# Performance work log

Hardware: AMD Instinct MI355X
Metric: run time of the kernel (lower is better)

Reference implementation:

```python
import jax, jax.numpy as jnp
import numpy as np

B, S, D, O, H, E, K = 4, 1024, 1024, 1024, 2048, 8, 2
EPS = 1e-5

def _layernorm(x, g, b):
    m = jnp.mean(x, axis=-1, keepdims=True)
    v = jnp.mean(jnp.square(x - m), axis=-1, keepdims=True)
    return (x - m) * jax.lax.rsqrt(v + EPS) * g + b

def setup_inputs() -> dict:
    key = jax.random.key(0)
    ks = jax.random.split(key, 8)
    def xavier(k, shape):
        fan_out, fan_in = shape[-2], shape[-1]
        bound = float(np.sqrt(6.0 / (fan_in + fan_out)))
        return jax.random.uniform(k, shape, jnp.float32, -bound, bound)
    return {
        "x": jax.random.normal(ks[0], (B, S, D), jnp.float32),
        "ln1_g": jnp.ones((D,), jnp.float32), "ln1_b": jnp.zeros((D,), jnp.float32),
        "router_w": xavier(ks[1], (E, D)), "router_b": jnp.zeros((E,), jnp.float32),
        "sh_w1": xavier(ks[2], (H, D)), "sh_b1": jnp.zeros((H,), jnp.float32),
        "sh_w2": xavier(ks[3], (O, H)), "sh_b2": jnp.zeros((O,), jnp.float32),
        "e_w1": xavier(ks[4], (E, H, D)), "e_b1": jnp.zeros((E, H), jnp.float32),
        "e_w2": xavier(ks[5], (E, O, H)), "e_b2": jnp.zeros((E, O), jnp.float32),
        "ln2_g": jnp.ones((O,), jnp.float32), "ln2_b": jnp.zeros((O,), jnp.float32),
    }

def reference(x, ln1_g, ln1_b, router_w, router_b, sh_w1, sh_b1, sh_w2, sh_b2,
              e_w1, e_b1, e_w2, e_b2, ln2_g, ln2_b):
    # eval mode: no router noise, no aux loss
    x_norm = _layernorm(x, ln1_g, ln1_b)               # [B,S,D]
    xf = x_norm.reshape(-1, D)                          # [T,D]
    logits = xf @ router_w.T + router_b                 # [T,E]
    probs = jax.nn.softmax(logits, axis=-1)
    tk_w, tk_i = jax.lax.top_k(probs, K)                # [T,K]
    tk_w = tk_w / jnp.sum(tk_w, axis=-1, keepdims=True)
    # shared expert (exact GELU, as torch nn.GELU default)
    shared = jax.nn.gelu(xf @ sh_w1.T + sh_b1, approximate=False) @ sh_w2.T + sh_b2  # [T,O]
    # all experts densely, combined sparsely by top-k weights
    hid = jax.nn.gelu(jnp.einsum('td,ehd->teh', xf, e_w1) + e_b1, approximate=False)  # [T,E,H]
    eout = jnp.einsum('teh,eoh->teo', hid, e_w2) + e_b2                                # [T,E,O]
    comb_w = jnp.sum(jax.nn.one_hot(tk_i, E, dtype=xf.dtype) * tk_w[..., None], axis=1)  # [T,E]
    out = shared * (1.0 / (E + 1)) + jnp.einsum('te,teo->to', comb_w, eout)           # [T,O]
    out = _layernorm(out.reshape(B, S, O), ln2_g, ln2_b)
    return out
```

## Files before the change

### kernel.cpp

```cpp
#include <hip/hip_runtime.h>
#include <math.h>
#include <stdint.h>

typedef unsigned short u16;
typedef unsigned int u32;

typedef __attribute__((ext_vector_type(8))) short bf16x8;
typedef __attribute__((ext_vector_type(4))) float f32x4;

#define ASYNC_COPY16(g, l)                                                         \
  __builtin_amdgcn_global_load_lds((__attribute__((address_space(1))) const void*)(g), \
                                   (__attribute__((address_space(3))) void*)(l), 16, 0, 0)

__device__ __forceinline__ float bf2f(u16 u) {
  union { u32 i; float f; } v; v.i = ((u32)u) << 16; return v.f;
}
__device__ __forceinline__ u16 f2bf(float f) {
  union { float f; u32 i; } v; v.f = f;
  u32 r = v.i + 0x7fffu + ((v.i >> 16) & 1u);
  return (u16)(r >> 16);
}

__global__ __launch_bounds__(256) void cvt_all_k(
    const float* __restrict__ s0, const float* __restrict__ s1,
    const float* __restrict__ s2, const float* __restrict__ s3,
    u16* __restrict__ dst)
{
  const int64_t i0 = (int64_t)blockIdx.x * 2048 + (int64_t)threadIdx.x * 8;
  const float* src; int64_t rel;
  if (i0 < 2097152)       { src = s0; rel = i0; }
  else if (i0 < 4194304)  { src = s1; rel = i0 - 2097152; }
  else if (i0 < 20971520) { src = s2; rel = i0 - 4194304; }
  else                    { src = s3; rel = i0 - 20971520; }
  const float4 a = *(const float4*)(src + rel);
  const float4 b = *(const float4*)(src + rel + 4);
  union { u16 h[8]; uint4 v; } o;
  o.h[0] = f2bf(a.x); o.h[1] = f2bf(a.y); o.h[2] = f2bf(a.z); o.h[3] = f2bf(a.w);
  o.h[4] = f2bf(b.x); o.h[5] = f2bf(b.y); o.h[6] = f2bf(b.z); o.h[7] = f2bf(b.w);
  *(uint4*)(dst + i0) = o.v;
}

__global__ __launch_bounds__(256) void ln_router_k(
    const float* __restrict__ x, const float* __restrict__ g, const float* __restrict__ b,
    const float* __restrict__ rw, const float* __restrict__ rb,
    u16* __restrict__ xn, int* __restrict__ tk_idx, float* __restrict__ tk_w)
{
  const int t = blockIdx.x, tid = threadIdx.x;
  __shared__ float xs[1024];
  __shared__ float red[8];
  __shared__ float logits[8];
  const int wave = tid >> 6, lane = tid & 63;

  const float4 xv = *(const float4*)(x + (size_t)t * 1024 + 4 * tid);
  float v0 = xv.x, v1 = xv.y, v2 = xv.z, v3 = xv.w;
  float s = v0 + v1 + v2 + v3;
  float q = v0 * v0 + v1 * v1 + v2 * v2 + v3 * v3;
#pragma unroll
  for (int o = 32; o > 0; o >>= 1) { s += __shfl_down(s, o, 64); q += __shfl_down(q, o, 64); }
  if (lane == 0) { red[wave] = s; red[4 + wave] = q; }
  __syncthreads();
  if (tid == 0) {
    float S = red[0] + red[1] + red[2] + red[3];
    float Q = red[4] + red[5] + red[6] + red[7];
    float mean = S * (1.0f / 1024.0f);
    float var = Q * (1.0f / 1024.0f) - mean * mean;
    red[0] = mean; red[1] = rsqrtf(var + 1e-5f);
  }
  __syncthreads();
  const float mean = red[0], rstd = red[1];
  float vv[4] = {v0, v1, v2, v3};
  union { u16 h[4]; uint2 v; } pk;
#pragma unroll
  for (int j = 0; j < 4; ++j) {
    int d = 4 * tid + j;
    float y = (vv[j] - mean) * rstd * g[d] + b[d];
    xs[d] = y;
    pk.h[j] = f2bf(y);
  }
  *(uint2*)(xn + (size_t)t * 1024 + 4 * tid) = pk.v;
  __syncthreads();
#pragma unroll
  for (int pe = 0; pe < 2; ++pe) {
    int e = wave + 4 * pe;
    const float* wrow = rw + (size_t)e * 1024;
    float acc = 0.f;
#pragma unroll
    for (int j = 0; j < 16; ++j) {
      int d = lane + 64 * j;
      acc += xs[d] * wrow[d];
    }
#pragma unroll
    for (int o = 32; o > 0; o >>= 1) acc += __shfl_down(acc, o, 64);
    if (lane == 0) logits[e] = acc + rb[e];
  }
  __syncthreads();
  if (tid == 0) {
    int i0 = 0; float l0 = logits[0];
#pragma unroll
    for (int e = 1; e < 8; ++e) if (logits[e] > l0) { l0 = logits[e]; i0 = e; }
    int i1 = -1; float l1 = -3.4e38f;
#pragma unroll
    for (int e = 0; e < 8; ++e) { if (e == i0) continue; if (logits[e] > l1) { l1 = logits[e]; i1 = e; } }
    float w0 = 1.0f / (1.0f + expf(l1 - l0));
    float w1 = 1.0f - w0;
    tk_idx[2 * t] = i0; tk_idx[2 * t + 1] = i1;
    tk_w[2 * t] = w0; tk_w[2 * t + 1] = w1;
  }
}

__device__ __forceinline__ uint4 u4_add(uint4 a, uint4 b) {
  uint4 r; r.x = a.x + b.x; r.y = a.y + b.y; r.z = a.z + b.z; r.w = a.w + b.w; return r;
}
__device__ __forceinline__ uint4 u4_sub(uint4 a, uint4 b) {
  uint4 r; r.x = a.x - b.x; r.y = a.y - b.y; r.z = a.z - b.z; r.w = a.w - b.w; return r;
}

__global__ __launch_bounds__(256) void assign_k(
    const int* __restrict__ tk_idx, const float* __restrict__ tk_w,
    int* __restrict__ offs, int* __restrict__ slot_token,
    float* __restrict__ slot_w, int* __restrict__ slot_of)
{
  const int tid = threadIdx.x, lane = tid & 63, wave = tid >> 6;
  int eidx[32];
#pragma unroll
  for (int j = 0; j < 32; ++j) eidx[j] = tk_idx[tid * 32 + j];

  uint4 p = {0u, 0u, 0u, 0u};
#pragma unroll
  for (int j = 0; j < 32; ++j) {
    int e = eidx[j];
    unsigned inc = 1u << ((e & 1) * 16);
    int c = e >> 1;
    if (c == 0) p.x += inc; else if (c == 1) p.y += inc;
    else if (c == 2) p.z += inc; else p.w += inc;
  }
  const uint4 own = p;
#pragma unroll
  for (int o = 1; o < 64; o <<= 1) {
    uint4 t;
    t.x = (u32)__shfl_up((int)p.x, o, 64);
    t.y = (u32)__shfl_up((int)p.y, o, 64);
    t.z = (u32)__shfl_up((int)p.z, o, 64);
    t.w = (u32)__shfl_up((int)p.w, o, 64);
    if (lane >= o) p = u4_add(p, t);
  }
  __shared__ uint4 wtot[4];
  __shared__ int offs_s[9];
  if (lane == 63) wtot[wave] = p;
  __syncthreads();
  uint4 wbase = {0u, 0u, 0u, 0u};
  uint4 gtot = {0u, 0u, 0u, 0u};
#pragma unroll
  for (int w2 = 0; w2 < 4; ++w2) {
    uint4 t = wtot[w2];
    if (w2 < wave) wbase = u4_add(wbase, t);
    gtot = u4_add(gtot, t);
  }
  const uint4 excl = u4_sub(p, own);
  if (tid == 0) {
    int gtots[8] = { (int)(gtot.x & 0xffff), (int)(gtot.x >> 16),
                     (int)(gtot.y & 0xffff), (int)(gtot.y >> 16),
                     (int)(gtot.z & 0xffff), (int)(gtot.z >> 16),
                     (int)(gtot.w & 0xffff), (int)(gtot.w >> 16) };
    int a = 0;
#pragma unroll
    for (int e = 0; e < 8; ++e) { offs_s[e] = a; offs[e] = a; a += gtots[e]; }
    offs_s[8] = a; offs[8] = a;
  }
  __syncthreads();
  const uint4 pre = u4_add(wbase, excl);
  int base[8];
  base[0] = offs_s[0] + (int)(pre.x & 0xffff);
  base[1] = offs_s[1] + (int)(pre.x >> 16);
  base[2] = offs_s[2] + (int)(pre.y & 0xffff);
  base[3] = offs_s[3] + (int)(pre.y >> 16);
  base[4] = offs_s[4] + (int)(pre.z & 0xffff);
  base[5] = offs_s[5] + (int)(pre.z >> 16);
  base[6] = offs_s[6] + (int)(pre.w & 0xffff);
  base[7] = offs_s[7] + (int)(pre.w >> 16);
#pragma unroll
  for (int j = 0; j < 32; ++j) {
    int idx = tid * 32 + j;
    int e = eidx[j];
    int s = base[e]++;
    slot_token[s] = idx >> 1;
    slot_w[s] = tk_w[idx];
    slot_of[idx] = s;
  }
}

template <int N, int KD, int STAGE>
__global__ __launch_bounds__(256) void gemm_fused_k(
    const u16* __restrict__ Abase, const u16* __restrict__ Bsh,
    const u16* __restrict__ Bex, const float* __restrict__ bias_sh,
    const float* __restrict__ bias_ex,
    float* __restrict__ outF, u16* __restrict__ outH,
    const int* __restrict__ offs, const int* __restrict__ slot_token,
    const float* __restrict__ slot_w)
{
  const int tid = threadIdx.x;
  const int z = blockIdx.z;
  int off = 0, cnt = 4096, obase = 0;
  const u16* B = Bsh;
  const float* biasp = bias_sh;
  if (z > 0) {
    off = offs[z - 1]; cnt = offs[z] - off; obase = 4096 + off;
    B = Bex + (size_t)(z - 1) * N * KD;
    biasp = bias_ex + (size_t)(z - 1) * N;
  }
  const int m0 = blockIdx.y * 128;
  if (m0 >= cnt) return;
  const int n0 = blockIdx.x * 128;

  __shared__ u16 lA[128 * 32];
  __shared__ u16 lB[128 * 32];

  const int rS = tid >> 2;
  const int c8 = (tid & 3) * 8;

  int ra0 = m0 + rS;      if (ra0 > cnt - 1) ra0 = cnt - 1;
  int ra1 = m0 + rS + 64; if (ra1 > cnt - 1) ra1 = cnt - 1;
  size_t arow0, arow1;
  if (STAGE == 1) {
    if (z == 0) { arow0 = (size_t)ra0; arow1 = (size_t)ra1; }
    else        { arow0 = (size_t)slot_token[off + ra0]; arow1 = (size_t)slot_token[off + ra1]; }
  } else {
    if (z == 0) { arow0 = (size_t)ra0; arow1 = (size_t)ra1; }
    else        { arow0 = (size_t)(4096 + off + ra0); arow1 = (size_t)(4096 + off + ra1); }
  }
  const u16* gA0 = Abase + arow0 * KD + c8;
  const u16* gA1 = Abase + arow1 * KD + c8;
  const u16* gB0 = B + (size_t)(n0 + rS) * KD + c8;
  const u16* gB1 = B + (size_t)(n0 + rS + 64) * KD + c8;

  const int wave = tid >> 6, lane = tid & 63;
  u16* lA_w0 = lA + wave * 512;
  u16* lA_w1 = lA + 2048 + wave * 512;
  u16* lB_w0 = lB + wave * 512;
  u16* lB_w1 = lB + 2048 + wave * 512;

  const int wr = wave >> 1, wc = wave & 1;
  const int fr = lane & 15, fq = lane >> 4;
  const u16* rdA = lA + (wr * 64 + fr) * 32 + fq * 8;
  const u16* rdB = lB + (wc * 64 + fr) * 32 + fq * 8;

  f32x4 acc[4][4];
  const f32x4 zero = {0.f, 0.f, 0.f, 0.f};
#pragma unroll
  for (int i = 0; i < 4; ++i)
#pragma unroll
    for (int n = 0; n < 4; ++n) acc[i][n] = zero;

  const int NK = KD / 32;
  for (int kb = 0; kb < NK; ++kb) {
    __syncthreads();
    ASYNC_COPY16(gA0, lA_w0);
    ASYNC_COPY16(gA1, lA_w1);
    ASYNC_COPY16(gB0, lB_w0);
    ASYNC_COPY16(gB1, lB_w1);
    gA0 += 32; gA1 += 32; gB0 += 32; gB1 += 32;
    __syncthreads();
    bf16x8 af[4], bfv[4];
#pragma unroll
    for (int i = 0; i < 4; ++i) af[i] = *(const bf16x8*)(rdA + i * 16 * 32);
#pragma unroll
    for (int n = 0; n < 4; ++n) bfv[n] = *(const bf16x8*)(rdB + n * 16 * 32);
#pragma unroll
    for (int i = 0; i < 4; ++i)
#pragma unroll
      for (int n = 0; n < 4; ++n)
        acc[i][n] = __builtin_amdgcn_mfma_f32_16x16x32_bf16(af[i], bfv[n], acc[i][n], 0, 0, 0);
  }

  const int colBase = n0 + wc * 64;
#pragma unroll
  for (int i = 0; i < 4; ++i) {
    const int mlBase = m0 + wr * 64 + i * 16 + fq * 4;
#pragma unroll
    for (int r = 0; r < 4; ++r) {
      const int ml = mlBase + r;
      if (ml >= cnt) continue;
      const size_t orow = (size_t)(obase + ml) * N;
      float rwgt = (STAGE == 2) ? ((z == 0) ? (1.0f / 9.0f) : slot_w[off + ml]) : 1.f;
#pragma unroll
      for (int n = 0; n < 4; ++n) {
        const int col = colBase + n * 16 + fr;
        float v = acc[i][n][r] + biasp[col];
        if (STAGE == 1) {
          v = 0.5f * v * (1.0f + erff(v * 0.70710678118654752f));
          outH[orow + col] = f2bf(v);
        } else {
          outF[orow + col] = v * rwgt;
        }
      }
    }
  }
}

__global__ __launch_bounds__(256) void combine_ln2_k(
    const float* __restrict__ sh_out, const float* __restrict__ eout,
    const int* __restrict__ slot_of,
    const float* __restrict__ g2, const float* __restrict__ b2,
    float* __restrict__ out)
{
  const int t = blockIdx.x, tid = threadIdx.x;
  const int wave = tid >> 6, lane = tid & 63;
  __shared__ float red[8];
  const size_t s0 = (size_t)slot_of[2 * t], s1 = (size_t)slot_of[2 * t + 1];
  const float4 a  = *(const float4*)(sh_out + (size_t)t * 1024 + 4 * tid);
  const float4 c0 = *(const float4*)(eout + s0 * 1024 + 4 * tid);
  const float4 c1 = *(const float4*)(eout + s1 * 1024 + 4 * tid);
  float v0 = a.x + c0.x + c1.x;
  float v1 = a.y + c0.y + c1.y;
  float v2 = a.z + c0.z + c1.z;
  float v3 = a.w + c0.w + c1.w;
  float s = v0 + v1 + v2 + v3;
  float q = v0 * v0 + v1 * v1 + v2 * v2 + v3 * v3;
#pragma unroll
  for (int o = 32; o > 0; o >>= 1) { s += __shfl_down(s, o, 64); q += __shfl_down(q, o, 64); }
  if (lane == 0) { red[wave] = s; red[4 + wave] = q; }
  __syncthreads();
  if (tid == 0) {
    float S = red[0] + red[1] + red[2] + red[3];
    float Q = red[4] + red[5] + red[6] + red[7];
    float mean = S * (1.0f / 1024.0f);
    float var = Q * (1.0f / 1024.0f) - mean * mean;
    red[0] = mean; red[1] = rsqrtf(var + 1e-5f);
  }
  __syncthreads();
  const float mean = red[0], rstd = red[1];
  float vv[4] = {v0, v1, v2, v3};
#pragma unroll
  for (int j = 0; j < 4; ++j) {
    int d = 4 * tid + j;
    out[(size_t)t * 1024 + d] = (vv[j] - mean) * rstd * g2[d] + b2[d];
  }
}

extern "C" void kernel_launch(void* const* d_in, const int* in_sizes, int n_in,
                              void* d_out, int out_size, void* d_ws, size_t ws_size,
                              hipStream_t stream)
{
  const float* x     = (const float*)d_in[0];
  const float* ln1_g = (const float*)d_in[1];
  const float* ln1_b = (const float*)d_in[2];
  const float* rw    = (const float*)d_in[3];
  const float* rb    = (const float*)d_in[4];
  const float* sh_w1 = (const float*)d_in[5];
  const float* sh_b1 = (const float*)d_in[6];
  const float* sh_w2 = (const float*)d_in[7];
  const float* sh_b2 = (const float*)d_in[8];
  const float* e_w1  = (const float*)d_in[9];
  const float* e_b1  = (const float*)d_in[10];
  const float* e_w2  = (const float*)d_in[11];
  const float* e_b2  = (const float*)d_in[12];
  const float* ln2_g = (const float*)d_in[13];
  const float* ln2_b = (const float*)d_in[14];
  float* out = (float*)d_out;

  char* w = (char*)d_ws;
  u16*   x_norm = (u16*)(w + 0);
  u16*   hid    = (u16*)(w + (8u << 20));
  float* outb   = (float*)(w + (56u << 20));
  u16*   w1b    = (u16*)(w + (104u << 20));
  u16*   w2b    = (u16*)(w + (108u << 20));
  u16*   ew1b   = (u16*)(w + (112u << 20));
  u16*   ew2b   = (u16*)(w + (144u << 20));
  char*  meta   = w + (176u << 20);
  int*   tk_idx     = (int*)(meta);
  float* tk_w       = (float*)(meta + (32u << 10));
  int*   slot_token = (int*)(meta + (64u << 10));
  float* slot_w     = (float*)(meta + (96u << 10));
  int*   slot_of    = (int*)(meta + (128u << 10));
  int*   offs       = (int*)(meta + (160u << 10));

  cvt_all_k<<<18432, 256, 0, stream>>>(sh_w1, sh_w2, e_w1, e_w2, w1b);

  ln_router_k<<<4096, 256, 0, stream>>>(x, ln1_g, ln1_b, rw, rb, x_norm, tk_idx, tk_w);
  assign_k<<<1, 256, 0, stream>>>(tk_idx, tk_w, offs, slot_token, slot_w, slot_of);

  gemm_fused_k<2048, 1024, 1><<<dim3(16, 32, 9), 256, 0, stream>>>(
      x_norm, w1b, ew1b, sh_b1, e_b1, nullptr, hid, offs, slot_token, nullptr);
  gemm_fused_k<1024, 2048, 2><<<dim3(8, 32, 9), 256, 0, stream>>>(
      hid, w2b, ew2b, sh_b2, e_b2, outb, nullptr, offs, slot_token, slot_w);

  combine_ln2_k<<<4096, 256, 0, stream>>>(outb, outb + (size_t)4096 * 1024,
                                          slot_of, ln2_g, ln2_b, out);
}
```

Before: 445.8 us.

## Double-buffer LDS tiles and store them in MFMA fragment order

The fused GEMM moves from a single LDS buffer with two barriers per k-step to a two-stage ping-pong buffer. The next k-tile's async global-to-LDS copies are issued before the current tile is read, so memory latency can overlap the MFMA work. The LDS tiles are also reordered so each wave's 16-row fragment is contiguous and every lane reads 16 consecutive bytes, which should cut bank conflicts on fragment loads. The cost is doubled LDS use, which may lower occupancy, and correctness now depends on the barrier covering completion of the async copies.

```diff
diff --git a/kernel.cpp b/kernel.cpp
--- a/kernel.cpp
+++ b/kernel.cpp
@@ -199,6 +199,8 @@
     const float* __restrict__ slot_w)
 {
   const int tid = threadIdx.x;
+  const int wave = tid >> 6, lane = tid & 63;
+  const int fr = lane & 15, fq = lane >> 4;
   const int z = blockIdx.z;
   int off = 0, cnt = 4096, obase = 0;
   const u16* B = Bsh;
@@ -212,37 +214,24 @@
   if (m0 >= cnt) return;
   const int n0 = blockIdx.x * 128;
 
-  __shared__ u16 lA[128 * 32];
-  __shared__ u16 lB[128 * 32];
-
-  const int rS = tid >> 2;
-  const int c8 = (tid & 3) * 8;
-
-  int ra0 = m0 + rS;      if (ra0 > cnt - 1) ra0 = cnt - 1;
-  int ra1 = m0 + rS + 64; if (ra1 > cnt - 1) ra1 = cnt - 1;
+  __shared__ u16 lds[2][8192];
+
+  int rowA0 = m0 + wave * 16 + fr;      if (rowA0 > cnt - 1) rowA0 = cnt - 1;
+  int rowA1 = m0 + 64 + wave * 16 + fr; if (rowA1 > cnt - 1) rowA1 = cnt - 1;
   size_t arow0, arow1;
   if (STAGE == 1) {
-    if (z == 0) { arow0 = (size_t)ra0; arow1 = (size_t)ra1; }
-    else        { arow0 = (size_t)slot_token[off + ra0]; arow1 = (size_t)slot_token[off + ra1]; }
+    if (z == 0) { arow0 = (size_t)rowA0; arow1 = (size_t)rowA1; }
+    else        { arow0 = (size_t)slot_token[off + rowA0]; arow1 = (size_t)slot_token[off + rowA1]; }
   } else {
-    if (z == 0) { arow0 = (size_t)ra0; arow1 = (size_t)ra1; }
-    else        { arow0 = (size_t)(4096 + off + ra0); arow1 = (size_t)(4096 + off + ra1); }
-  }
-  const u16* gA0 = Abase + arow0 * KD + c8;
-  const u16* gA1 = Abase + arow1 * KD + c8;
-  const u16* gB0 = B + (size_t)(n0 + rS) * KD + c8;
-  const u16* gB1 = B + (size_t)(n0 + rS + 64) * KD + c8;
-
-  const int wave = tid >> 6, lane = tid & 63;
-  u16* lA_w0 = lA + wave * 512;
-  u16* lA_w1 = lA + 2048 + wave * 512;
-  u16* lB_w0 = lB + wave * 512;
-  u16* lB_w1 = lB + 2048 + wave * 512;
+    if (z == 0) { arow0 = (size_t)rowA0; arow1 = (size_t)rowA1; }
+    else        { arow0 = (size_t)(4096 + off + rowA0); arow1 = (size_t)(4096 + off + rowA1); }
+  }
+  const u16* gA0 = Abase + arow0 * KD + fq * 8;
+  const u16* gA1 = Abase + arow1 * KD + fq * 8;
+  const u16* gB0 = B + (size_t)(n0 + wave * 16 + fr) * KD + fq * 8;
+  const u16* gB1 = B + (size_t)(n0 + 64 + wave * 16 + fr) * KD + fq * 8;
 
   const int wr = wave >> 1, wc = wave & 1;
-  const int fr = lane & 15, fq = lane >> 4;
-  const u16* rdA = lA + (wr * 64 + fr) * 32 + fq * 8;
-  const u16* rdB = lB + (wc * 64 + fr) * 32 + fq * 8;
 
   f32x4 acc[4][4];
   const f32x4 zero = {0.f, 0.f, 0.f, 0.f};
@@ -252,19 +241,32 @@
     for (int n = 0; n < 4; ++n) acc[i][n] = zero;
 
   const int NK = KD / 32;
+  {
+    u16* nb = &lds[0][0];
+    ASYNC_COPY16(gA0, nb + wave * 512);
+    ASYNC_COPY16(gA1, nb + (4 + wave) * 512);
+    ASYNC_COPY16(gB0, nb + 4096 + wave * 512);
+    ASYNC_COPY16(gB1, nb + 4096 + (4 + wave) * 512);
+    gA0 += 32; gA1 += 32; gB0 += 32; gB1 += 32;
+  }
+
   for (int kb = 0; kb < NK; ++kb) {
+    const int cur = kb & 1;
     __syncthreads();
-    ASYNC_COPY16(gA0, lA_w0);
-    ASYNC_COPY16(gA1, lA_w1);
-    ASYNC_COPY16(gB0, lB_w0);
-    ASYNC_COPY16(gB1, lB_w1);
-    gA0 += 32; gA1 += 32; gB0 += 32; gB1 += 32;
-    __syncthreads();
+    if (kb + 1 < NK) {
+      u16* nb = &lds[cur ^ 1][0];
+      ASYNC_COPY16(gA0, nb + wave * 512);
+      ASYNC_COPY16(gA1, nb + (4 + wave) * 512);
+      ASYNC_COPY16(gB0, nb + 4096 + wave * 512);
+      ASYNC_COPY16(gB1, nb + 4096 + (4 + wave) * 512);
+      gA0 += 32; gA1 += 32; gB0 += 32; gB1 += 32;
+    }
+    const u16* cb = &lds[cur][0];
     bf16x8 af[4], bfv[4];
 #pragma unroll
-    for (int i = 0; i < 4; ++i) af[i] = *(const bf16x8*)(rdA + i * 16 * 32);
-#pragma unroll
-    for (int n = 0; n < 4; ++n) bfv[n] = *(const bf16x8*)(rdB + n * 16 * 32);
+    for (int i = 0; i < 4; ++i) af[i] = *(const bf16x8*)(cb + (wr * 4 + i) * 512 + lane * 8);
+#pragma unroll
+    for (int n = 0; n < 4; ++n) bfv[n] = *(const bf16x8*)(cb + 4096 + (wc * 4 + n) * 512 + lane * 8);
 #pragma unroll
     for (int i = 0; i < 4; ++i)
 #pragma unroll
```

After: 508.8 us. 14.1% more time.
